# Kernel tuning notes

Hardware: AMD Instinct MI355X
Metric: run time of the kernel (lower is better)

Reference implementation:

```python
import jax, jax.numpy as jnp
import numpy as np

B = 8; A = 9; NUM_CLASSES = 80
BRANCH_HW = [(80, 80), (40, 40)]; STRIDES = [8, 16]
IMG_H, IMG_W = 640, 640
CLASS_OFFSETS = [0, 0]
SCORE_THR = 0.05; NMS_THR = 0.5; MARGIN = 0.0
PRE_NMS = 1000; POST_NMS = 300
MIN_H, MIN_W = 0.0, 0.0
BBOX_CLIP = float(np.log(1000.0 / 16.0))  # torchvision-style dw/dh clamp


def _make_anchors(H, W, stride):
    # A square anchors per cell, grid-aligned (x1,y1,x2,y2)
    sizes = np.array([16., 32., 64., 20., 40., 80., 24., 48., 96.])[:A]
    cx = (np.arange(W) + 0.5) * stride
    cy = (np.arange(H) + 0.5) * stride
    cy_g, cx_g = np.meshgrid(cy, cx, indexing='ij')  # [H,W]
    half = sizes / 2.0  # [A]
    x1 = cx_g[..., None] - half; y1 = cy_g[..., None] - half
    x2 = cx_g[..., None] + half; y2 = cy_g[..., None] + half
    anc = np.stack([x1, y1, x2, y2], -1).astype(np.float32)  # [H,W,A,4]
    anc = anc.reshape(H, W, A * 4).transpose(2, 0, 1)  # [A*4,H,W]
    return jnp.asarray(np.broadcast_to(anc[None], (B,) + anc.shape).copy())


def setup_inputs() -> dict:
    key = jax.random.key(0)
    ks = jax.random.split(key, 2)
    out = {}
    for i, (Hh, Ww) in enumerate(BRANCH_HW):
        d = jax.random.normal(ks[i], (B, Hh, Ww, A, 4 + NUM_CLASSES), jnp.float32)
        d = d.at[..., :4].multiply(0.25)  # keep box deltas in a sane range
        out['data%d' % i] = d.reshape(B, Hh, Ww, A * (4 + NUM_CLASSES)).transpose(0, 3, 1, 2)
        out['anchors%d' % i] = _make_anchors(Hh, Ww, STRIDES[i])
    return out


def _unfold(t, d):
    b = t.shape[0]
    return jnp.transpose(t, (0, 2, 3, 1)).reshape(b, -1, d)


def _decode(deltas, anchors):
    # BoxCoder((1,1,1,1)).decode_single
    aw = anchors[..., 2] - anchors[..., 0]; ah = anchors[..., 3] - anchors[..., 1]
    acx = anchors[..., 0] + 0.5 * aw; acy = anchors[..., 1] + 0.5 * ah
    dx, dy, dw, dh = (deltas[..., 0], deltas[..., 1], deltas[..., 2], deltas[..., 3])
    pcx = dx * aw + acx; pcy = dy * ah + acy
    pw = jnp.exp(jnp.minimum(dw, BBOX_CLIP)) * aw
    ph = jnp.exp(jnp.minimum(dh, BBOX_CLIP)) * ah
    return jnp.stack([pcx - 0.5 * pw, pcy - 0.5 * ph, pcx + 0.5 * pw, pcy + 0.5 * ph], -1)


def _iou(b):
    area = (b[:, 2] - b[:, 0]) * (b[:, 3] - b[:, 1])
    lt = jnp.maximum(b[:, None, :2], b[None, :, :2])
    rb = jnp.minimum(b[:, None, 2:], b[None, :, 2:])
    wh = jnp.clip(rb - lt, 0.0)
    inter = wh[..., 0] * wh[..., 1]
    return inter / (area[:, None] + area[None, :] - inter + 1e-9)


def _nms_single(boxes, cls, scores):
    # sort by score, take pre_nms_top_k
    sc, idx = jax.lax.top_k(scores, PRE_NMS)
    b = boxes[idx]; c = cls[idx]
    # score threshold + min-hw validity filter (masked instead of dynamic slice)
    valid = (sc >= SCORE_THR) & (b[:, 0] < b[:, 2] - MIN_W) & (b[:, 1] < b[:, 3] - MIN_H)
    iou = _iou(b)  # [PRE,PRE]
    rng = jnp.arange(PRE_NMS)

    def body(i, keep):
        # box j suppressed by kept box i if IoU>thr and score_i - score_j > margin
        sup = keep[i] & (iou[i] > NMS_THR) & ((sc[i] - sc) > MARGIN) & (rng > i)
        return keep & (~sup)

    keep = jax.lax.fori_loop(0, PRE_NMS, body, valid)
    # kept boxes first (score order preserved), then pad_zero to POST_NMS
    order = jnp.argsort(jnp.where(keep, rng, rng + PRE_NMS))[:POST_NMS]
    km = keep[order]
    return (jnp.where(km[:, None], b[order], 0.0),
            jnp.where(km, sc[order], 0.0),
            jnp.where(km, c[order], 0.0))


def reference(data0, data1, anchors0, anchors1):
    datas = [data0, data1]; ancs = [anchors0, anchors1]
    fa, deltas, scores, offs = [], [], [], []
    for i in range(2):
        fa.append(_unfold(ancs[i], 4))
        u = _unfold(datas[i], 4 + NUM_CLASSES)
        deltas.append(u[..., :4]); scores.append(u[..., 4:])
        offs.append(jnp.full((1, u.shape[1]), float(CLASS_OFFSETS[i]), jnp.float32))
    fa = jnp.concatenate(fa, 1); deltas = jnp.concatenate(deltas, 1)
    scores = jnp.concatenate(scores, 1); offs = jnp.concatenate(offs, 1)
    max_sc = scores.max(-1)
    cls = jnp.argmax(scores, -1).astype(jnp.float32) + offs
    boxes = _decode(deltas, fa)
    # clip to image
    x = jnp.clip(boxes[..., 0::2], 0.0, float(IMG_W))
    y = jnp.clip(boxes[..., 1::2], 0.0, float(IMG_H))
    boxes = jnp.stack([x[..., 0], y[..., 0], x[..., 1], y[..., 1]], -1)
    return jax.vmap(_nms_single)(boxes, cls, max_sc)  # ([B,POST,4],[B,POST],[B,POST])
```

## Files before the change

kernel.cpp:

```cpp
#include <hip/hip_runtime.h>
#include <math.h>

#pragma clang fp contract(off)

#define BB      8
#define AA      9
#define NCLS    80
#define NTOT    72000
#define PRE     1000
#define POST    300
#define CAP     4096
#define BCLIP   4.135166556742356f
#define NBLK0   1440
#define NBLK1   360
#define DS1BASE 1843200

__device__ __constant__ float c_sizes[9] = {16.f,32.f,64.f,20.f,40.f,80.f,24.f,48.f,96.f};

__device__ inline unsigned fkey(float s) {
    unsigned u = __float_as_uint(s);
    return (u & 0x80000000u) ? ~u : (u | 0x80000000u);
}
__device__ inline float unfkey(unsigned u) {
    return __uint_as_float((u & 0x80000000u) ? (u ^ 0x80000000u) : ~u);
}

template<int BR>
__device__ inline void stream_impl(int bx, const float* __restrict__ data,
                                   unsigned long long* __restrict__ partial,
                                   float* __restrict__ dstage,
                                   unsigned long long* lkey)
{
    constexpr int ROWF4 = BR ? 400 : 1600;
    int slab, cg, hwq;
    if (BR == 0) { slab = bx / 20; int r = bx % 20; cg = r / 4; hwq = r % 4; }
    else         { slab = bx / 5;  cg = bx % 5;  hwq = 0; }
    int b = slab / 9, a = slab - (slab / 9) * 9;
    int nch = cg ? 16 : 20;
    int c_first = cg ? (4 + cg * 16) : 0;

    for (int i = threadIdx.x; i < 1600; i += 256) lkey[i] = 0ULL;
    __syncthreads();

    const float4* d4 = (const float4*)data;
    size_t rowbase = (size_t)(b * 756 + a * 84 + c_first) * ROWF4 + hwq * 400;
    float4* ds4 = (float4*)dstage;

    int tid = threadIdx.x;
    int rr2 = tid + 256;
    bool s2 = (rr2 < 400);

    for (int c0 = 0; c0 < nch; c0 += 4) {
        float4 v[8];
        #pragma unroll
        for (int u = 0; u < 4; u++) {
            size_t base = rowbase + (size_t)(c0 + u) * ROWF4;
            v[2 * u]     = d4[base + tid];
            v[2 * u + 1] = s2 ? d4[base + rr2] : make_float4(0.f, 0.f, 0.f, 0.f);
        }
        #pragma unroll
        for (int u = 0; u < 4; u++) {
            int ch = c_first + c0 + u;
            if (ch < 4) {
                size_t di0, di1;
                if (BR) { di0 = (size_t)(DS1BASE / 4) + (size_t)(slab * 4 + ch) * 400 + tid;
                          di1 = di0 + 256; }
                else    { di0 = (size_t)(slab * 4 + ch) * 1600 + hwq * 400 + tid;
                          di1 = di0 + 256; }
                ds4[di0] = v[2 * u];
                if (s2) ds4[di1] = v[2 * u + 1];
            } else {
                unsigned icls = ~(unsigned)(ch - 4);
                float4 x = v[2 * u];
                int cell = tid * 4;
                atomicMax(&lkey[cell + 0], ((unsigned long long)fkey(x.x) << 32) | icls);
                atomicMax(&lkey[cell + 1], ((unsigned long long)fkey(x.y) << 32) | icls);
                atomicMax(&lkey[cell + 2], ((unsigned long long)fkey(x.z) << 32) | icls);
                atomicMax(&lkey[cell + 3], ((unsigned long long)fkey(x.w) << 32) | icls);
                if (s2) {
                    float4 y = v[2 * u + 1];
                    int cell2 = rr2 * 4;
                    atomicMax(&lkey[cell2 + 0], ((unsigned long long)fkey(y.x) << 32) | icls);
                    atomicMax(&lkey[cell2 + 1], ((unsigned long long)fkey(y.y) << 32) | icls);
                    atomicMax(&lkey[cell2 + 2], ((unsigned long long)fkey(y.z) << 32) | icls);
                    atomicMax(&lkey[cell2 + 3], ((unsigned long long)fkey(y.w) << 32) | icls);
                }
            }
        }
    }
    __syncthreads();

    size_t pbase = (size_t)cg * 576000 + (size_t)b * 72000
                 + (BR ? (size_t)(57600 + a * 1600) : (size_t)(a * 6400 + hwq * 1600));
    for (int cell = threadIdx.x; cell < 1600; cell += 256)
        partial[pbase + cell] = lkey[cell];
}

__global__ __launch_bounds__(256) void k_stream(
    const float* __restrict__ data0, const float* __restrict__ data1,
    unsigned long long* __restrict__ partial, float* __restrict__ dstage)
{
    __shared__ unsigned long long lkey[1600];
    int bx = blockIdx.x;
    if (bx < NBLK0) stream_impl<0>(bx, data0, partial, dstage, lkey);
    else            stream_impl<1>(bx - NBLK0, data1, partial, dstage, lkey);
}

__global__ __launch_bounds__(256) void k_cells(
    const unsigned long long* __restrict__ partial, const float* __restrict__ dstage,
    float* __restrict__ boxes, float* __restrict__ scores, float* __restrict__ cls,
    unsigned* __restrict__ chist)
{
    __shared__ unsigned lh[256];
    int tid = threadIdx.x;
    lh[tid] = 0;
    __syncthreads();

    int b = blockIdx.y;
    int mm = blockIdx.x * 256 + tid;
    if (mm < 36000) {
        const ulonglong2* p2 = (const ulonglong2*)partial;
        ulonglong2 best = p2[(size_t)b * 36000 + mm];
        #pragma unroll
        for (int g = 1; g < 5; g++) {
            ulonglong2 v = p2[(size_t)g * 288000 + (size_t)b * 36000 + mm];
            if (v.x > best.x) best.x = v.x;
            if (v.y > best.y) best.y = v.y;
        }
        unsigned long long kk[2] = { best.x, best.y };

        int m0 = mm * 2;
        int a, hw, W, STRIDE;
        size_t dbase;
        if (m0 < 57600) {
            a = m0 / 6400; hw = m0 - a * 6400; W = 80; STRIDE = 8;
            dbase = (size_t)((b * 9 + a) * 4) * 6400 + hw;
        } else {
            int m1 = m0 - 57600;
            a = m1 / 1600; hw = m1 - a * 1600; W = 40; STRIDE = 16;
            dbase = (size_t)DS1BASE + (size_t)((b * 9 + a) * 4) * 1600 + hw;
        }
        size_t cstride = (m0 < 57600) ? 6400 : 1600;
        float2 dx = *(const float2*)(dstage + dbase);
        float2 dy = *(const float2*)(dstage + dbase + cstride);
        float2 dw = *(const float2*)(dstage + dbase + 2 * cstride);
        float2 dh = *(const float2*)(dstage + dbase + 3 * cstride);
        float dxa[2] = {dx.x, dx.y}, dya[2] = {dy.x, dy.y};
        float dwa[2] = {dw.x, dw.y}, dha[2] = {dh.x, dh.y};

        float sz = c_sizes[a];
        size_t o = (size_t)b * NTOT + m0;

        #pragma unroll
        for (int k = 0; k < 2; k++) {
            int hwk = hw + k;
            int h = hwk / W;
            int w = hwk - h * W;
            float cy = (h + 0.5f) * (float)STRIDE;
            float cx = (w + 0.5f) * (float)STRIDE;
            float pcx = dxa[k] * sz + cx;
            float pcy = dya[k] * sz + cy;
            float pw  = expf(fminf(dwa[k], BCLIP)) * sz;
            float ph  = expf(fminf(dha[k], BCLIP)) * sz;
            float x1 = fminf(fmaxf(pcx - 0.5f * pw, 0.f), 640.f);
            float y1 = fminf(fmaxf(pcy - 0.5f * ph, 0.f), 640.f);
            float x2 = fminf(fmaxf(pcx + 0.5f * pw, 0.f), 640.f);
            float y2 = fminf(fmaxf(pcy + 0.5f * ph, 0.f), 640.f);
            ((float4*)boxes)[o + k] = make_float4(x1, y1, x2, y2);
            scores[o + k] = unfkey((unsigned)(kk[k] >> 32));
            cls[o + k]    = (float)(~(unsigned)kk[k]);
            atomicAdd(&lh[(unsigned)(kk[k] >> 56)], 1u);
        }
    }
    __syncthreads();
    if (lh[tid]) atomicAdd(&chist[b * 256 + tid], lh[tid]);
}

__global__ __launch_bounds__(256) void k_cscan(const unsigned* __restrict__ chist,
                                               unsigned* __restrict__ Cca)
{
    __shared__ unsigned S[256];
    int b = blockIdx.x, tid = threadIdx.x;
    S[tid] = chist[b * 256 + tid];
    __syncthreads();
    for (int off = 1; off < 256; off <<= 1) {
        unsigned v = S[tid] + ((tid + off < 256) ? S[tid + off] : 0u);
        __syncthreads();
        S[tid] = v;
        __syncthreads();
    }
    if (S[tid] >= (unsigned)PRE && (tid == 255 || S[tid + 1] < (unsigned)PRE)) {
        Cca[b * 2]     = (unsigned)tid;
        Cca[b * 2 + 1] = (tid == 255) ? 0u : S[tid + 1];
    }
}

__global__ __launch_bounds__(256) void k_fine(const float* __restrict__ scores,
                                              const unsigned* __restrict__ Cca,
                                              unsigned* __restrict__ fhist)
{
    __shared__ unsigned lh[256];
    int tid = threadIdx.x;
    lh[tid] = 0;
    __syncthreads();
    int b = blockIdx.y;
    unsigned C = Cca[b * 2];
    int m4 = blockIdx.x * 256 + tid;
    if (m4 < NTOT / 4) {
        float sv[4];
        *(float4*)sv = ((const float4*)(scores + (size_t)b * NTOT))[m4];
        #pragma unroll
        for (int k = 0; k < 4; k++) {
            unsigned u = fkey(sv[k]);
            if ((u >> 24) == C) atomicAdd(&lh[(u >> 16) & 0xFF], 1u);
        }
    }
    __syncthreads();
    if (lh[tid]) atomicAdd(&fhist[b * 256 + tid], lh[tid]);
}

__global__ __launch_bounds__(256) void k_fthr(const unsigned* __restrict__ fhist,
                                              const unsigned* __restrict__ Cca,
                                              unsigned* __restrict__ T)
{
    __shared__ unsigned S[256];
    int b = blockIdx.x, tid = threadIdx.x;
    unsigned C = Cca[b * 2], ca = Cca[b * 2 + 1];
    S[tid] = fhist[b * 256 + tid];
    __syncthreads();
    for (int off = 1; off < 256; off <<= 1) {
        unsigned v = S[tid] + ((tid + off < 256) ? S[tid + off] : 0u);
        __syncthreads();
        S[tid] = v;
        __syncthreads();
    }
    if (ca + S[tid] >= (unsigned)PRE && (tid == 255 || ca + S[tid + 1] < (unsigned)PRE))
        T[b] = (C << 8) | (unsigned)tid;
}

__global__ __launch_bounds__(256) void k_compact(const float* __restrict__ scores,
                                                 const unsigned* __restrict__ T,
                                                 unsigned* __restrict__ cnt,
                                                 unsigned long long* __restrict__ cand)
{
    int m4 = blockIdx.x * 256 + threadIdx.x;
    int b = blockIdx.y;
    if (m4 >= NTOT / 4) return;
    float sv[4];
    *(float4*)sv = ((const float4*)(scores + (size_t)b * NTOT))[m4];
    unsigned Tb = T[b];
    #pragma unroll
    for (int k = 0; k < 4; k++) {
        unsigned u = fkey(sv[k]);
        if ((u >> 16) >= Tb) {
            int m = m4 * 4 + k;
            int n;
            if (m < 57600) { int a = m / 6400; int hw = m - a * 6400; n = hw * 9 + a; }
            else { int mm = m - 57600; int a = mm / 1600; int hw = mm - a * 1600; n = 57600 + hw * 9 + a; }
            unsigned pos = atomicAdd(&cnt[b], 1u);
            if (pos < CAP)
                cand[(size_t)b * CAP + pos] = ((unsigned long long)u << 32) | (unsigned)(~(unsigned)n);
        }
    }
}

__global__ __launch_bounds__(1024) void k_sort(
    const unsigned long long* __restrict__ cand, const unsigned* __restrict__ cnt,
    const float* __restrict__ boxes, const float* __restrict__ scores, const float* __restrict__ cls,
    float* __restrict__ sboxes, float* __restrict__ sscores, float* __restrict__ scls)
{
    __shared__ unsigned long long keys[CAP];
    int b = blockIdx.x, tid = threadIdx.x;
    int c = min((int)cnt[b], CAP);
    int P = 1024;
    while (P < c) P <<= 1;
    for (int i = tid; i < P; i += 1024)
        keys[i] = (i < c) ? cand[(size_t)b * CAP + i] : 0ULL;

    for (int k2 = 2; k2 <= P; k2 <<= 1)
        for (int j = k2 >> 1; j > 0; j >>= 1) {
            __syncthreads();
            for (int i = tid; i < P; i += 1024) {
                int l = i ^ j;
                if (l > i) {
                    unsigned long long x = keys[i], y = keys[l];
                    bool up = ((i & k2) == 0);
                    if ((x > y) == up) { keys[i] = y; keys[l] = x; }
                }
            }
        }
    __syncthreads();

    if (tid < PRE) {
        unsigned long long key = keys[P - 1 - tid];
        int n = (int)~(unsigned)(key & 0xFFFFFFFFu);
        int m;
        if (n < 57600) { int hw = n / 9; int a = n - hw * 9; m = a * 6400 + hw; }
        else { int n2 = n - 57600; int hw = n2 / 9; int a = n2 - hw * 9; m = 57600 + a * 1600 + hw; }
        size_t src = (size_t)b * NTOT + m;
        ((float4*)sboxes)[b * 1024 + tid] = ((const float4*)boxes)[src];
        sscores[b * 1024 + tid] = scores[src];
        scls[b * 1024 + tid] = cls[src];
    }
}

__global__ __launch_bounds__(1024) void k_mask(const float* __restrict__ sboxes,
                                               const float* __restrict__ sscores,
                                               unsigned long long* __restrict__ mask)
{
    __shared__ float4 bx[64];
    __shared__ float  sl[64];
    int b = blockIdx.y, w = blockIdx.x, tid = threadIdx.x;
    if (tid < 64) {
        int j = w * 64 + tid;
        bx[tid] = ((const float4*)sboxes)[b * 1024 + j];
        sl[tid] = sscores[b * 1024 + j];
    }
    __syncthreads();
    int r = tid;
    unsigned long long* dst = &mask[((size_t)(b * 1024) + r) * 16 + w];
    if (r >= PRE || w * 64 + 63 <= r) { *dst = 0ULL; return; }

    float4 br = ((const float4*)sboxes)[b * 1024 + r];
    float sr = sscores[b * 1024 + r];
    float arear = (br.z - br.x) * (br.w - br.y);
    unsigned long long bits = 0;
    int jend = min(64, PRE - w * 64);
    for (int jj = 0; jj < jend; jj++) {
        int j = w * 64 + jj;
        float4 bj = bx[jj];
        float ix1 = fmaxf(br.x, bj.x), iy1 = fmaxf(br.y, bj.y);
        float ix2 = fminf(br.z, bj.z), iy2 = fminf(br.w, bj.w);
        float iw = fmaxf(ix2 - ix1, 0.f), ih = fmaxf(iy2 - iy1, 0.f);
        float inter = iw * ih;
        float areaj = (bj.z - bj.x) * (bj.w - bj.y);
        float iou = inter / (arear + areaj - inter + 1e-9f);
        if (j > r && iou > 0.5f && sr > sl[jj]) bits |= 1ull << jj;
    }
    *dst = bits;
}

__global__ __launch_bounds__(64) void k_nms(const unsigned long long* __restrict__ mask,
                                            const float* __restrict__ sboxes,
                                            const float* __restrict__ sscores,
                                            const float* __restrict__ scls,
                                            float* __restrict__ out)
{
    int b = blockIdx.x, lane = threadIdx.x;
    const unsigned long long* mrow = mask + (size_t)b * 1024 * 16;

    unsigned long long validw = 0;
    for (int w = 0; w < 16; w++) {
        int r = w * 64 + lane;
        bool v = false;
        if (r < PRE) {
            float sc = sscores[b * 1024 + r];
            float4 bbx = ((const float4*)sboxes)[b * 1024 + r];
            v = (sc >= 0.05f) && (bbx.x < bbx.z) && (bbx.y < bbx.w);
        }
        unsigned long long bal = __ballot(v);
        if (lane == w) validw = bal;
    }

    unsigned long long remv = 0, keepw = 0;

    for (int c = 0; c < 16; c++) {
        const unsigned long long* myrow = mrow + (size_t)(c * 64 + lane) * 16;
        unsigned long long m_cc = myrow[c];
        unsigned long long rw[16];
        rw[0] = 0;
        #pragma unroll
        for (int w = 1; w < 16; w++)
            rw[w] = (w > c) ? myrow[w] : 0ULL;

        unsigned long long cur = __shfl(validw & ~remv, c);
        unsigned long long todo = cur;
        while (todo) {
            int jj = __ffsll((unsigned long long)todo) - 1;
            unsigned long long row = __shfl(m_cc, jj);
            cur &= ~row;
            todo = (todo & (todo - 1)) & ~row;
        }
        if (lane == c) keepw = cur;

        bool mykept = ((cur >> lane) & 1ULL) != 0;
        #pragma unroll
        for (int w = 1; w < 16; w++) {
            if (w > c) {
                unsigned long long v = mykept ? rw[w] : 0ULL;
                v |= __shfl_xor(v, 32);
                v |= __shfl_xor(v, 16);
                v |= __shfl_xor(v, 8);
                v |= __shfl_xor(v, 4);
                v |= __shfl_xor(v, 2);
                v |= __shfl_xor(v, 1);
                if (lane == w) remv |= v;
            }
        }
    }

    __shared__ unsigned long long kws[16];
    __shared__ int pfx[17];
    if (lane < 16) kws[lane] = keepw;
    __syncthreads();
    if (lane == 0) {
        int s = 0;
        for (int w = 0; w < 16; w++) { pfx[w] = s; s += __popcll(kws[w]); }
        pfx[16] = s;
    }
    __syncthreads();
    int nk = pfx[16];

    float* ob = out;
    float* os = out + BB * POST * 4;
    float* oc = os + BB * POST;

    for (int r = lane; r < PRE; r += 64) {
        int w = r >> 6;
        unsigned long long kw = kws[w];
        if ((kw >> (r & 63)) & 1ULL) {
            int rank = pfx[w] + __popcll(kw & ((1ULL << (r & 63)) - 1ULL));
            if (rank < POST) {
                ((float4*)ob)[b * POST + rank] = ((const float4*)sboxes)[b * 1024 + r];
                os[b * POST + rank] = sscores[b * 1024 + r];
                oc[b * POST + rank] = scls[b * 1024 + r];
            }
        }
    }
    for (int p = nk + lane; p < POST; p += 64) {
        ((float4*)ob)[b * POST + p] = make_float4(0.f, 0.f, 0.f, 0.f);
        os[b * POST + p] = 0.f;
        oc[b * POST + p] = 0.f;
    }
}

extern "C" void kernel_launch(void* const* d_in, const int* in_sizes, int n_in,
                              void* d_out, int out_size, void* d_ws, size_t ws_size,
                              hipStream_t stream)
{
    const float* data0 = (const float*)d_in[0];
    const float* data1 = (const float*)d_in[2];
    for (int i = 0; i < n_in; i++) {
        if (in_sizes[i] == 8 * 756 * 6400) data0 = (const float*)d_in[i];
        else if (in_sizes[i] == 8 * 756 * 1600) data1 = (const float*)d_in[i];
    }

    char* ws = (char*)d_ws;
    size_t off = 0;
    auto alloc = [&](size_t bytes) -> char* {
        char* p = ws + off;
        off = (off + bytes + 255) & ~(size_t)255;
        return p;
    };

    float* boxes   = (float*)alloc((size_t)BB * NTOT * 4 * 4);
    float* scores  = (float*)alloc((size_t)BB * NTOT * 4);
    float* cls     = (float*)alloc((size_t)BB * NTOT * 4);
    unsigned* cnt   = (unsigned*)alloc(BB * 4);
    unsigned* chist = (unsigned*)alloc(BB * 256 * 4);
    unsigned* fhist = (unsigned*)alloc(BB * 256 * 4);
    unsigned* Cca  = (unsigned*)alloc(BB * 2 * 4);
    unsigned* T    = (unsigned*)alloc(BB * 4);
    unsigned long long* cand = (unsigned long long*)alloc((size_t)BB * CAP * 8);
    float* sboxes  = (float*)alloc((size_t)BB * 1024 * 4 * 4);
    float* sscores = (float*)alloc((size_t)BB * 1024 * 4);
    float* scls    = (float*)alloc((size_t)BB * 1024 * 4);
    unsigned long long* mask = (unsigned long long*)alloc((size_t)BB * 1024 * 16 * 8);
    unsigned long long* partial = (unsigned long long*)alloc((size_t)5 * 576000 * 8);
    float* dstage  = (float*)alloc((size_t)(DS1BASE + 72 * 4 * 1600) * 4);

    (void)hipMemsetAsync(cnt, 0, 256 + 2 * (size_t)BB * 256 * 4, stream);

    k_stream<<<NBLK0 + NBLK1, 256, 0, stream>>>(data0, data1, partial, dstage);

    dim3 gc(141, BB);
    k_cells<<<gc, 256, 0, stream>>>(partial, dstage, boxes, scores, cls, chist);

    k_cscan<<<BB, 256, 0, stream>>>(chist, Cca);
    dim3 gf((NTOT / 4 + 255) / 256, BB);
    k_fine<<<gf, 256, 0, stream>>>(scores, Cca, fhist);
    k_fthr<<<BB, 256, 0, stream>>>(fhist, Cca, T);

    k_compact<<<gf, 256, 0, stream>>>(scores, T, cnt, cand);

    k_sort<<<BB, 1024, 0, stream>>>(cand, cnt, boxes, scores, cls, sboxes, sscores, scls);

    dim3 g5(16, BB);
    k_mask<<<g5, 1024, 0, stream>>>(sboxes, sscores, mask);

    k_nms<<<BB, 64, 0, stream>>>(mask, sboxes, sscores, scls, (float*)d_out);
}
```

Before: 498.1 us.

## Transpose NMS suppression mask to column layout and use ballot-based greedy scan

The suppression mask is now stored per column (which earlier boxes suppress box j) in a transposed layout, so each lane reads coalesced words for its own box. The serial NMS kernel no longer OR-reduces suppression rows across the wavefront with shuffle trees. Instead each lane ANDs its column words with the kept bitmasks of earlier chunks, and resolves the diagonal chunk with a ballot loop. This removes many shuffles from the latency-bound single-wavefront kernel, in exchange for keeping 16 kept-words per lane in registers.

```diff
diff --git a/kernel.cpp b/kernel.cpp
--- a/kernel.cpp
+++ b/kernel.cpp
@@ -306,106 +306,94 @@
 
 __global__ __launch_bounds__(1024) void k_mask(const float* __restrict__ sboxes,
                                                const float* __restrict__ sscores,
-                                               unsigned long long* __restrict__ mask)
+                                               unsigned long long* __restrict__ maskT)
 {
     __shared__ float4 bx[64];
     __shared__ float  sl[64];
     int b = blockIdx.y, w = blockIdx.x, tid = threadIdx.x;
     if (tid < 64) {
-        int j = w * 64 + tid;
-        bx[tid] = ((const float4*)sboxes)[b * 1024 + j];
-        sl[tid] = sscores[b * 1024 + j];
-    }
-    __syncthreads();
-    int r = tid;
-    unsigned long long* dst = &mask[((size_t)(b * 1024) + r) * 16 + w];
-    if (r >= PRE || w * 64 + 63 <= r) { *dst = 0ULL; return; }
-
-    float4 br = ((const float4*)sboxes)[b * 1024 + r];
-    float sr = sscores[b * 1024 + r];
-    float arear = (br.z - br.x) * (br.w - br.y);
+        int i = w * 64 + tid;
+        bx[tid] = ((const float4*)sboxes)[b * 1024 + i];
+        sl[tid] = sscores[b * 1024 + i];
+    }
+    __syncthreads();
+    int j = tid;
+    unsigned long long* dst = &maskT[((size_t)(b * 16) + w) * 1024 + j];
+    if (j >= PRE || w * 64 >= j) { *dst = 0ULL; return; }
+
+    float4 bj = ((const float4*)sboxes)[b * 1024 + j];
+    float sj = sscores[b * 1024 + j];
+    float areaj = (bj.z - bj.x) * (bj.w - bj.y);
     unsigned long long bits = 0;
-    int jend = min(64, PRE - w * 64);
-    for (int jj = 0; jj < jend; jj++) {
-        int j = w * 64 + jj;
-        float4 bj = bx[jj];
-        float ix1 = fmaxf(br.x, bj.x), iy1 = fmaxf(br.y, bj.y);
-        float ix2 = fminf(br.z, bj.z), iy2 = fminf(br.w, bj.w);
+    int iend = min(64, j - w * 64);
+    for (int ii = 0; ii < iend; ii++) {
+        float4 bi = bx[ii];
+        float ix1 = fmaxf(bi.x, bj.x), iy1 = fmaxf(bi.y, bj.y);
+        float ix2 = fminf(bi.z, bj.z), iy2 = fminf(bi.w, bj.w);
         float iw = fmaxf(ix2 - ix1, 0.f), ih = fmaxf(iy2 - iy1, 0.f);
         float inter = iw * ih;
-        float areaj = (bj.z - bj.x) * (bj.w - bj.y);
-        float iou = inter / (arear + areaj - inter + 1e-9f);
-        if (j > r && iou > 0.5f && sr > sl[jj]) bits |= 1ull << jj;
+        float areai = (bi.z - bi.x) * (bi.w - bi.y);
+        float iou = inter / (areai + areaj - inter + 1e-9f);
+        if (iou > 0.5f && sl[ii] > sj) bits |= 1ull << ii;
     }
     *dst = bits;
 }
 
-__global__ __launch_bounds__(64) void k_nms(const unsigned long long* __restrict__ mask,
+__global__ __launch_bounds__(64) void k_nms(const unsigned long long* __restrict__ maskT,
                                             const float* __restrict__ sboxes,
                                             const float* __restrict__ sscores,
                                             const float* __restrict__ scls,
                                             float* __restrict__ out)
 {
     int b = blockIdx.x, lane = threadIdx.x;
-    const unsigned long long* mrow = mask + (size_t)b * 1024 * 16;
-
-    unsigned long long validw = 0;
-    for (int w = 0; w < 16; w++) {
-        int r = w * 64 + lane;
+    const unsigned long long* base = maskT + (size_t)b * 16 * 1024;
+
+    unsigned validbits = 0;
+    #pragma unroll
+    for (int c = 0; c < 16; c++) {
+        int r = c * 64 + lane;
         bool v = false;
         if (r < PRE) {
             float sc = sscores[b * 1024 + r];
             float4 bbx = ((const float4*)sboxes)[b * 1024 + r];
             v = (sc >= 0.05f) && (bbx.x < bbx.z) && (bbx.y < bbx.w);
         }
-        unsigned long long bal = __ballot(v);
-        if (lane == w) validw = bal;
-    }
-
-    unsigned long long remv = 0, keepw = 0;
-
+        validbits |= (v ? 1u : 0u) << c;
+    }
+
+    unsigned long long keptw[16];
+    #pragma unroll
     for (int c = 0; c < 16; c++) {
-        const unsigned long long* myrow = mrow + (size_t)(c * 64 + lane) * 16;
-        unsigned long long m_cc = myrow[c];
-        unsigned long long rw[16];
-        rw[0] = 0;
-        #pragma unroll
-        for (int w = 1; w < 16; w++)
-            rw[w] = (w > c) ? myrow[w] : 0ULL;
-
-        unsigned long long cur = __shfl(validw & ~remv, c);
-        unsigned long long todo = cur;
-        while (todo) {
-            int jj = __ffsll((unsigned long long)todo) - 1;
-            unsigned long long row = __shfl(m_cc, jj);
-            cur &= ~row;
-            todo = (todo & (todo - 1)) & ~row;
-        }
-        if (lane == c) keepw = cur;
-
-        bool mykept = ((cur >> lane) & 1ULL) != 0;
-        #pragma unroll
-        for (int w = 1; w < 16; w++) {
-            if (w > c) {
-                unsigned long long v = mykept ? rw[w] : 0ULL;
-                v |= __shfl_xor(v, 32);
-                v |= __shfl_xor(v, 16);
-                v |= __shfl_xor(v, 8);
-                v |= __shfl_xor(v, 4);
-                v |= __shfl_xor(v, 2);
-                v |= __shfl_xor(v, 1);
-                if (lane == w) remv |= v;
-            }
-        }
+        unsigned long long acc = 0, col = 0;
+        #pragma unroll
+        for (int w = 0; w <= c; w++) {
+            unsigned long long m = base[(w << 10) + c * 64 + lane];
+            if (w < c) acc |= m & keptw[w];
+            else       col = m;
+        }
+        bool alive = (((validbits >> c) & 1u) != 0u) && (acc == 0ULL);
+
+        unsigned long long ab = __ballot(alive);
+        unsigned long long kw = 0;
+        while (ab) {
+            int f = __ffsll((unsigned long long)ab) - 1;
+            kw |= 1ULL << f;
+            alive = alive && (lane != f) && (((col >> f) & 1ULL) == 0ULL);
+            ab = __ballot(alive);
+        }
+        keptw[c] = kw;
     }
 
     __shared__ unsigned long long kws[16];
     __shared__ int pfx[17];
-    if (lane < 16) kws[lane] = keepw;
-    __syncthreads();
     if (lane == 0) {
         int s = 0;
-        for (int w = 0; w < 16; w++) { pfx[w] = s; s += __popcll(kws[w]); }
+        #pragma unroll
+        for (int w = 0; w < 16; w++) {
+            kws[w] = keptw[w];
+            pfx[w] = s;
+            s += __popcll(keptw[w]);
+        }
         pfx[16] = s;
     }
     __syncthreads();
@@ -465,7 +453,7 @@
     float* sboxes  = (float*)alloc((size_t)BB * 1024 * 4 * 4);
     float* sscores = (float*)alloc((size_t)BB * 1024 * 4);
     float* scls    = (float*)alloc((size_t)BB * 1024 * 4);
-    unsigned long long* mask = (unsigned long long*)alloc((size_t)BB * 1024 * 16 * 8);
+    unsigned long long* maskT = (unsigned long long*)alloc((size_t)BB * 16 * 1024 * 8);
     unsigned long long* partial = (unsigned long long*)alloc((size_t)5 * 576000 * 8);
     float* dstage  = (float*)alloc((size_t)(DS1BASE + 72 * 4 * 1600) * 4);
 
@@ -486,7 +474,7 @@
     k_sort<<<BB, 1024, 0, stream>>>(cand, cnt, boxes, scores, cls, sboxes, sscores, scls);
 
     dim3 g5(16, BB);
-    k_mask<<<g5, 1024, 0, stream>>>(sboxes, sscores, mask);
-
-    k_nms<<<BB, 64, 0, stream>>>(mask, sboxes, sscores, scls, (float*)d_out);
-}
+    k_mask<<<g5, 1024, 0, stream>>>(sboxes, sscores, maskT);
+
+    k_nms<<<BB, 64, 0, stream>>>(maskT, sboxes, sscores, scls, (float*)d_out);
+}
```

Measured after the change: 458.0 us. -8.1%, faster.
